# Kernel optimization log

Hardware: AMD Instinct MI355X
Metric: run time of the kernel (lower is better)

## Reference

```python
import jax, jax.numpy as jnp
import numpy as np

B = 1_000_000   # reflections
K = 16_384      # groups
E = 64          # encoder_out
H = 64          # hidden_dim


def setup_inputs() -> dict:
    key = jax.random.key(0)
    ks = jax.random.split(key, 12)
    x = jax.random.normal(ks[0], (B, E), dtype=jnp.float32)
    gl = jax.random.randint(ks[1], (B,), 0, K)
    # guarantee every group id 0..K-1 appears, so torch.unique == arange(K)
    gl = gl.at[:K].set(jnp.arange(K))
    s = 0.05
    W1 = jax.random.normal(ks[2], (E, H), jnp.float32) * s
    b1 = jax.random.normal(ks[3], (H,), jnp.float32) * s
    W2 = jax.random.normal(ks[4], (H, H), jnp.float32) * s
    b2 = jax.random.normal(ks[5], (H,), jnp.float32) * s
    W3 = jax.random.normal(ks[6], (H, H), jnp.float32) * s
    b3 = jax.random.normal(ks[7], (H,), jnp.float32) * s
    w_mu = jax.random.normal(ks[8], (H, 1), jnp.float32) * s
    b_mu = jnp.full((1,), -6.9, jnp.float32)   # log_tau_init
    w_lv = jax.random.normal(ks[9], (H, 1), jnp.float32) * s
    b_lv = jnp.full((1,), -2.0, jnp.float32)
    return {"x": x, "group_labels": gl, "W1": W1, "b1": b1, "W2": W2, "b2": b2,
            "W3": W3, "b3": b3, "w_mu": w_mu, "b_mu": b_mu, "w_lv": w_lv, "b_lv": b_lv}


def reference(x, group_labels, W1, b1, W2, b2, W3, b3, w_mu, b_mu, w_lv, b_lv):
    # phi: Linear -> SiLU -> Linear -> SiLU
    z = jax.nn.silu(jax.nn.silu(x @ W1 + b1) @ W2 + b2)          # (B, H)
    # segment mean by group (math-equivalent to the dense one-hot matmul)
    counts = jax.ops.segment_sum(jnp.ones((z.shape[0],), z.dtype),
                                 group_labels, num_segments=K)    # (K,)
    gsum = jax.ops.segment_sum(z, group_labels, num_segments=K)   # (K, H)
    group_features = gsum / counts[:, None]
    # rho + heads
    h = jax.nn.silu(group_features @ W3 + b3)                     # (K, H)
    mu = (h @ w_mu + b_mu)[:, 0]                                  # (K,)
    logvar = jnp.clip((h @ w_lv + b_lv)[:, 0], -10.0, 4.0)        # (K,)
    std = jnp.exp(0.5 * logvar)
    eps = jax.random.normal(jax.random.key(42), std.shape, std.dtype)
    log_tau = mu + std * eps                                      # reparam sample
    tau_group = jnp.exp(log_tau)
    # unique_groups == arange(K) by construction -> searchsorted is identity
    tau_per_refl = tau_group[group_labels][:, None]               # (B, 1)
    log_tau_per_refl = log_tau[group_labels][:, None]             # (B, 1)
    return (mu, logvar, tau_per_refl, log_tau_per_refl)
```

## Files before the change

kernel.cpp:

```cpp
#include <hip/hip_runtime.h>

#define BN 1000000
#define KN 16384
#define HN 64

typedef __bf16 bf16x8 __attribute__((ext_vector_type(8)));
typedef float  f32x4  __attribute__((ext_vector_type(4)));
typedef unsigned short u16x8 __attribute__((ext_vector_type(8)));

__device__ __forceinline__ unsigned short f2bf(float f) {
    unsigned u = __float_as_uint(f);
    u += 0x7fffu + ((u >> 16) & 1u);
    return (unsigned short)(u >> 16);
}
__device__ __forceinline__ float bf2f(unsigned short b) {
    return __uint_as_float(((unsigned)b) << 16);
}
__device__ __forceinline__ float silu_f(float v) {
    return v * __builtin_amdgcn_rcpf(1.0f + __expf(-v));
}
__device__ __forceinline__ f32x4 mfma16(bf16x8 a, bf16x8 b, f32x4 c) {
    return __builtin_amdgcn_mfma_f32_16x16x32_bf16(a, b, c, 0, 0, 0);
}

__device__ __forceinline__ float erfinv_xla(float x) {
    float w = -log1pf(-x * x);
    float p;
    if (w < 5.0f) {
        w -= 2.5f;
        p = 2.81022636e-08f;
        p = fmaf(p, w, 3.43273939e-07f);
        p = fmaf(p, w, -3.5233877e-06f);
        p = fmaf(p, w, -4.39150654e-06f);
        p = fmaf(p, w, 0.00021858087f);
        p = fmaf(p, w, -0.00125372503f);
        p = fmaf(p, w, -0.00417768164f);
        p = fmaf(p, w, 0.246640727f);
        p = fmaf(p, w, 1.50140941f);
    } else {
        w = sqrtf(w) - 3.0f;
        p = -0.000200214257f;
        p = fmaf(p, w, 0.000100950558f);
        p = fmaf(p, w, 0.00134934322f);
        p = fmaf(p, w, -0.00367342844f);
        p = fmaf(p, w, 0.00573950773f);
        p = fmaf(p, w, -0.0076224613f);
        p = fmaf(p, w, 0.00943887047f);
        p = fmaf(p, w, 1.00167406f);
        p = fmaf(p, w, 2.83297682f);
    }
    return p * x;
}

__device__ __forceinline__ float jax_eps16384(int gid) {
    const unsigned k0 = 0u, k1 = 42u, k2 = 0x1BD11BDAu ^ 0u ^ 42u;
    unsigned x0 = 0u + k0;
    unsigned x1 = (unsigned)gid + k1;
#define TF_RND(r) { x0 += x1; x1 = (x1 << (r)) | (x1 >> (32 - (r))); x1 ^= x0; }
    TF_RND(13) TF_RND(15) TF_RND(26) TF_RND(6)  x0 += k1; x1 += k2 + 1u;
    TF_RND(17) TF_RND(29) TF_RND(16) TF_RND(24) x0 += k2; x1 += k0 + 2u;
    TF_RND(13) TF_RND(15) TF_RND(26) TF_RND(6)  x0 += k0; x1 += k1 + 3u;
    TF_RND(17) TF_RND(29) TF_RND(16) TF_RND(24) x0 += k1; x1 += k2 + 4u;
    TF_RND(13) TF_RND(15) TF_RND(26) TF_RND(6)  x0 += k2; x1 += k0 + 5u;
#undef TF_RND
    unsigned bits = x0 ^ x1;
    float f = __uint_as_float((bits >> 9) | 0x3f800000u) - 1.0f;
    const float mn = -0.99999994f;
    float u = fmaxf(f * 2.0f + mn, mn);
    return 1.41421354f * erfinv_xla(u);
}

__global__ __launch_bounds__(256) void k_count(const int* __restrict__ gl, int* __restrict__ counts) {
    int i = blockIdx.x * 256 + threadIdx.x;
    if (i < BN) atomicAdd(&counts[gl[i]], 1);
}

__global__ __launch_bounds__(1024) void k_scan(const int* __restrict__ counts, int* __restrict__ cursor) {
    __shared__ int part[1024];
    int t = threadIdx.x;
    int loc[16]; int s = 0;
    #pragma unroll
    for (int i = 0; i < 16; ++i) { loc[i] = s; s += counts[t * 16 + i]; }
    part[t] = s;
    __syncthreads();
    for (int off = 1; off < 1024; off <<= 1) {
        int v = (t >= off) ? part[t - off] : 0;
        __syncthreads();
        part[t] += v;
        __syncthreads();
    }
    int base = (t > 0) ? part[t - 1] : 0;
    #pragma unroll
    for (int i = 0; i < 16; ++i) cursor[t * 16 + i] = base + loc[i];
}

__global__ __launch_bounds__(256) void k_scatter(const int* __restrict__ gl, int* __restrict__ cursor,
                                                 int2* __restrict__ spk) {
    int i = blockIdx.x * 256 + threadIdx.x;
    if (i < BN) {
        int g = gl[i];
        int p = atomicAdd(&cursor[g], 1);
        spk[p] = make_int2(i, g);
    }
}

__global__ __launch_bounds__(256) void k_phase1(
    const float* __restrict__ x, const int2* __restrict__ spk,
    const float* __restrict__ W1, const float* __restrict__ b1,
    const float* __restrict__ W2, const float* __restrict__ b2,
    float* __restrict__ gsum)
{
    __shared__ __align__(16) unsigned short w1t[64 * 64];
    __shared__ __align__(16) unsigned short w2t[64 * 64];
    __shared__ __align__(16) unsigned short xh[4][64 * 64];
    __shared__ float b1s[64], b2s[64];
    __shared__ __align__(16) int sg_s[256];

    const int t = threadIdx.x;
    const int base = blockIdx.x * 256;
    const int t4 = t >> 4;
    const int kc = (t & 15) * 4;

    int   rid0[8];
    float4 xv0[8];
    #pragma unroll
    for (int i = 0; i < 8; ++i) {
        int r = base + i * 16 + t4;
        rid0[i] = (r < BN) ? spk[r].x : -1;
    }
    #pragma unroll
    for (int i = 0; i < 8; ++i)
        xv0[i] = (rid0[i] >= 0) ? *(const float4*)(x + (size_t)rid0[i] * 64 + kc)
                                : make_float4(0.f, 0.f, 0.f, 0.f);

    {
        const float4* W1v = (const float4*)W1;
        const float4* W2v = (const float4*)W2;
        #pragma unroll
        for (int i = 0; i < 4; ++i) {
            int e4 = i * 256 + t;
            int k  = e4 >> 4;
            int j0 = (e4 & 15) * 4;
            float4 a = W1v[e4];
            float4 b = W2v[e4];
            float av[4] = {a.x, a.y, a.z, a.w};
            float bv[4] = {b.x, b.y, b.z, b.w};
            #pragma unroll
            for (int c = 0; c < 4; ++c) {
                int j = j0 + c;
                int off = j * 128 + ((2 * k) ^ ((j & 7) << 4));
                *(unsigned short*)((char*)w1t + off) = f2bf(av[c]);
                *(unsigned short*)((char*)w2t + off) = f2bf(bv[c]);
            }
        }
    }

    #pragma unroll
    for (int i = 0; i < 8; ++i) {
        int rr = i * 16 + t4;
        int w = rr >> 6, lr = rr & 63;
        int off = lr * 128 + ((2 * kc) ^ ((lr & 7) << 4));
        ushort4 pk;
        pk.x = f2bf(xv0[i].x); pk.y = f2bf(xv0[i].y);
        pk.z = f2bf(xv0[i].z); pk.w = f2bf(xv0[i].w);
        *(ushort4*)((char*)&xh[w][0] + off) = pk;
    }

    int   rid1[8];
    float4 xv1[8];
    #pragma unroll
    for (int i = 0; i < 8; ++i) {
        int r = base + (8 + i) * 16 + t4;
        rid1[i] = (r < BN) ? spk[r].x : -1;
    }
    #pragma unroll
    for (int i = 0; i < 8; ++i)
        xv1[i] = (rid1[i] >= 0) ? *(const float4*)(x + (size_t)rid1[i] * 64 + kc)
                                : make_float4(0.f, 0.f, 0.f, 0.f);

    if (t < 64) { b1s[t] = b1[t]; b2s[t] = b2[t]; }
    {
        int r = base + t;
        sg_s[t] = (r < BN) ? spk[r].y : -1;
    }

    #pragma unroll
    for (int i = 0; i < 8; ++i) {
        int rr = (8 + i) * 16 + t4;
        int w = rr >> 6, lr = rr & 63;
        int off = lr * 128 + ((2 * kc) ^ ((lr & 7) << 4));
        ushort4 pk;
        pk.x = f2bf(xv1[i].x); pk.y = f2bf(xv1[i].y);
        pk.z = f2bf(xv1[i].z); pk.w = f2bf(xv1[i].w);
        *(ushort4*)((char*)&xh[w][0] + off) = pk;
    }
    __syncthreads();

    const int wv = t >> 6, lane = t & 63;
    const int lj = lane & 15, lg = lane >> 4;
    unsigned short* myx = &xh[wv][0];

    f32x4 acc[4][4];
    #pragma unroll
    for (int a = 0; a < 4; ++a)
        #pragma unroll
        for (int b = 0; b < 4; ++b) acc[a][b] = f32x4{0.f, 0.f, 0.f, 0.f};

    #pragma unroll
    for (int kk = 0; kk < 2; ++kk) {
        const int kbyte = kk * 64 + lg * 16;
        bf16x8 bw[4];
        #pragma unroll
        for (int ct = 0; ct < 4; ++ct) {
            int row = ct * 16 + lj;
            bw[ct] = *(const bf16x8*)((char*)w1t + row * 128 + (kbyte ^ ((row & 7) << 4)));
        }
        #pragma unroll
        for (int rt = 0; rt < 4; ++rt) {
            int row = rt * 16 + lj;
            bf16x8 aw = *(const bf16x8*)((char*)myx + row * 128 + (kbyte ^ ((row & 7) << 4)));
            #pragma unroll
            for (int ct = 0; ct < 4; ++ct)
                acc[rt][ct] = mfma16(aw, bw[ct], acc[rt][ct]);
        }
    }
    {
        float bc[4];
        #pragma unroll
        for (int ct = 0; ct < 4; ++ct) bc[ct] = b1s[ct * 16 + lj];
        #pragma unroll
        for (int rt = 0; rt < 4; ++rt) {
            #pragma unroll
            for (int ct = 0; ct < 4; ++ct) {
                f32x4 v = acc[rt][ct];
                #pragma unroll
                for (int rg = 0; rg < 4; ++rg) {
                    int row = rt * 16 + lg * 4 + rg;
                    int col = ct * 16 + lj;
                    float h = silu_f(v[rg] + bc[ct]);
                    int off = row * 128 + ((2 * col) ^ ((row & 7) << 4));
                    *(unsigned short*)((char*)myx + off) = f2bf(h);
                }
                acc[rt][ct] = f32x4{0.f, 0.f, 0.f, 0.f};
            }
        }
    }
    __syncthreads();

    #pragma unroll
    for (int kk = 0; kk < 2; ++kk) {
        const int kbyte = kk * 64 + lg * 16;
        bf16x8 bw[4];
        #pragma unroll
        for (int ct = 0; ct < 4; ++ct) {
            int row = ct * 16 + lj;
            bw[ct] = *(const bf16x8*)((char*)w2t + row * 128 + (kbyte ^ ((row & 7) << 4)));
        }
        #pragma unroll
        for (int rt = 0; rt < 4; ++rt) {
            int row = rt * 16 + lj;
            bf16x8 aw = *(const bf16x8*)((char*)myx + row * 128 + (kbyte ^ ((row & 7) << 4)));
            #pragma unroll
            for (int ct = 0; ct < 4; ++ct)
                acc[rt][ct] = mfma16(aw, bw[ct], acc[rt][ct]);
        }
    }
    {
        float bc[4];
        #pragma unroll
        for (int ct = 0; ct < 4; ++ct) bc[ct] = b2s[ct * 16 + lj];
        #pragma unroll
        for (int rt = 0; rt < 4; ++rt) {
            #pragma unroll
            for (int ct = 0; ct < 4; ++ct) {
                f32x4 v = acc[rt][ct];
                int col  = ct * 16 + lj;
                int row0 = rt * 16 + lg * 4;
                ushort4 pk;
                pk.x = f2bf(silu_f(v[0] + bc[ct]));
                pk.y = f2bf(silu_f(v[1] + bc[ct]));
                pk.z = f2bf(silu_f(v[2] + bc[ct]));
                pk.w = f2bf(silu_f(v[3] + bc[ct]));
                *(ushort4*)((char*)myx + col * 128 + ((2 * row0) ^ ((col & 7) << 4))) = pk;
            }
        }
    }

    {
        const int c  = t & 63;
        const int ch = t >> 6;
        const char* zT = (const char*)&xh[ch][0];
        float vsum = 0.0f;
        int curg = -2;
        #pragma unroll
        for (int blk = 0; blk < 8; ++blk) {
            u16x8 v = *(const u16x8*)(zT + c * 128 + ((16 * blk) ^ ((c & 7) << 4)));
            int4 ga = *(const int4*)(&sg_s[ch * 64 + blk * 8]);
            int4 gb = *(const int4*)(&sg_s[ch * 64 + blk * 8 + 4]);
            int gs[8] = {ga.x, ga.y, ga.z, ga.w, gb.x, gb.y, gb.z, gb.w};
            #pragma unroll
            for (int j = 0; j < 8; ++j) {
                int g = gs[j];
                if (g != curg) {
                    if (curg >= 0) atomicAdd(&gsum[curg * 64 + c], vsum);
                    vsum = 0.0f;
                    curg = g;
                }
                vsum += bf2f(v[j]);
            }
        }
        if (curg >= 0) atomicAdd(&gsum[curg * 64 + c], vsum);
    }
}

__global__ __launch_bounds__(64) void k_phase2(
    const float* __restrict__ gsum, const int* __restrict__ counts,
    const float* __restrict__ W3, const float* __restrict__ b3,
    const float* __restrict__ wmu, const float* __restrict__ bmu,
    const float* __restrict__ wlv, const float* __restrict__ blv,
    float* __restrict__ out, float* __restrict__ taug, float* __restrict__ ltaug)
{
    __shared__ __align__(16) float w3t[64 * 64];
    __shared__ float b3s[64], wmus[64], wlvs[64];
    const int t = threadIdx.x;
    for (int i = 0; i < 64; ++i) w3t[t * 64 + i] = W3[i * 64 + t];
    b3s[t] = b3[t]; wmus[t] = wmu[t]; wlvs[t] = wlv[t];
    __syncthreads();

    const int gid = blockIdx.x * 64 + t;
    const float inv = 1.0f / (float)counts[gid];
    float gf[64];
    #pragma unroll
    for (int i = 0; i < 16; ++i) {
        float4 v = *(const float4*)(gsum + (size_t)gid * 64 + i * 4);
        gf[i * 4 + 0] = v.x * inv; gf[i * 4 + 1] = v.y * inv;
        gf[i * 4 + 2] = v.z * inv; gf[i * 4 + 3] = v.w * inv;
    }
    float mu = bmu[0], lv = blv[0];
    for (int j = 0; j < 64; ++j) {
        float a = b3s[j];
        const float4* wr = (const float4*)(w3t + j * 64);
        #pragma unroll
        for (int k = 0; k < 16; ++k) {
            float4 wv = wr[k];
            a += gf[k * 4 + 0] * wv.x + gf[k * 4 + 1] * wv.y
               + gf[k * 4 + 2] * wv.z + gf[k * 4 + 3] * wv.w;
        }
        float h = silu_f(a);
        mu += h * wmus[j];
        lv += h * wlvs[j];
    }
    lv = fminf(fmaxf(lv, -10.0f), 4.0f);
    float sd  = __expf(0.5f * lv);
    float eps = jax_eps16384(gid);
    float lt  = mu + sd * eps;
    out[gid]      = mu;
    out[KN + gid] = lv;
    taug[gid]  = __expf(lt);
    ltaug[gid] = lt;
}

__global__ __launch_bounds__(256) void k_phase3(
    const int* __restrict__ gl, const float* __restrict__ taug,
    const float* __restrict__ ltaug, float* __restrict__ out)
{
    int i = blockIdx.x * 256 + threadIdx.x;
    if (i < BN) {
        int g = gl[i];
        out[2 * KN + i]      = taug[g];
        out[2 * KN + BN + i] = ltaug[g];
    }
}

extern "C" void kernel_launch(void* const* d_in, const int* in_sizes, int n_in,
                              void* d_out, int out_size, void* d_ws, size_t ws_size,
                              hipStream_t stream)
{
    const float* x   = (const float*)d_in[0];
    const int*   gl  = (const int*)d_in[1];
    const float* W1  = (const float*)d_in[2];
    const float* b1  = (const float*)d_in[3];
    const float* W2  = (const float*)d_in[4];
    const float* b2  = (const float*)d_in[5];
    const float* W3  = (const float*)d_in[6];
    const float* b3  = (const float*)d_in[7];
    const float* wmu = (const float*)d_in[8];
    const float* bmu = (const float*)d_in[9];
    const float* wlv = (const float*)d_in[10];
    const float* blv = (const float*)d_in[11];
    float* out = (float*)d_out;

    float* ws     = (float*)d_ws;
    float* gsum   = ws;
    int*   counts = (int*)(gsum + KN * HN);
    int*   cursor = counts + KN;
    float* taug   = (float*)(cursor + KN);
    float* ltaug  = taug + KN;
    int2*  spk    = (int2*)(ltaug + KN);

    hipMemsetAsync(gsum, 0, (size_t)KN * HN * sizeof(float), stream);
    hipMemsetAsync(counts, 0, (size_t)KN * sizeof(int), stream);

    const int nb = (BN + 255) / 256;
    k_count  <<<nb, 256, 0, stream>>>(gl, counts);
    k_scan   <<<1, 1024, 0, stream>>>(counts, cursor);
    k_scatter<<<nb, 256, 0, stream>>>(gl, cursor, spk);
    k_phase1 <<<nb, 256, 0, stream>>>(x, spk, W1, b1, W2, b2, gsum);
    k_phase2 <<<KN / 64, 64, 0, stream>>>(gsum, counts, W3, b3, wmu, bmu, wlv, blv, out, taug, ltaug);
    k_phase3 <<<nb, 256, 0, stream>>>(gl, taug, ltaug, out);
}
```

Before: 241.9 us.

## Vectorize index kernels, fold gsum zeroing, load A fragments directly in phase1

```diff
diff --git a/kernel.cpp b/kernel.cpp
--- a/kernel.cpp
+++ b/kernel.cpp
@@ -3,6 +3,8 @@
 #define BN 1000000
 #define KN 16384
 #define HN 64
+#define TPB 384
+#define NW  6
 
 typedef __bf16 bf16x8 __attribute__((ext_vector_type(8)));
 typedef float  f32x4  __attribute__((ext_vector_type(4)));
@@ -70,41 +72,65 @@
     return 1.41421354f * erfinv_xla(u);
 }
 
-__global__ __launch_bounds__(256) void k_count(const int* __restrict__ gl, int* __restrict__ counts) {
+__global__ __launch_bounds__(256) void k_count(const int* __restrict__ gl,
+                                               int* __restrict__ counts,
+                                               float4* __restrict__ gz) {
     int i = blockIdx.x * 256 + threadIdx.x;
-    if (i < BN) atomicAdd(&counts[gl[i]], 1);
+    const float4 z4 = make_float4(0.f, 0.f, 0.f, 0.f);
+    for (int j = i; j < KN * HN / 4; j += 250112) gz[j] = z4;
+    if (i < BN / 4) {
+        int4 g = ((const int4*)gl)[i];
+        atomicAdd(&counts[g.x], 1); atomicAdd(&counts[g.y], 1);
+        atomicAdd(&counts[g.z], 1); atomicAdd(&counts[g.w], 1);
+    }
 }
 
 __global__ __launch_bounds__(1024) void k_scan(const int* __restrict__ counts, int* __restrict__ cursor) {
-    __shared__ int part[1024];
-    int t = threadIdx.x;
-    int loc[16]; int s = 0;
-    #pragma unroll
-    for (int i = 0; i < 16; ++i) { loc[i] = s; s += counts[t * 16 + i]; }
-    part[t] = s;
+    __shared__ int wtot[16];
+    const int t = threadIdx.x, lane = t & 63, wv = t >> 6;
+    const int4* c4 = (const int4*)counts;
+    int4 q0 = c4[t * 4], q1 = c4[t * 4 + 1], q2 = c4[t * 4 + 2], q3 = c4[t * 4 + 3];
+    int c[16] = {q0.x, q0.y, q0.z, q0.w, q1.x, q1.y, q1.z, q1.w,
+                 q2.x, q2.y, q2.z, q2.w, q3.x, q3.y, q3.z, q3.w};
+    int loc[16], s = 0;
+    #pragma unroll
+    for (int i = 0; i < 16; ++i) { loc[i] = s; s += c[i]; }
+    const int own = s;
+    #pragma unroll
+    for (int off = 1; off < 64; off <<= 1) {
+        int v = __shfl_up(s, off);
+        if (lane >= off) s += v;
+    }
+    if (lane == 63) wtot[wv] = s;
     __syncthreads();
-    for (int off = 1; off < 1024; off <<= 1) {
-        int v = (t >= off) ? part[t - off] : 0;
-        __syncthreads();
-        part[t] += v;
-        __syncthreads();
-    }
-    int base = (t > 0) ? part[t - 1] : 0;
-    #pragma unroll
-    for (int i = 0; i < 16; ++i) cursor[t * 16 + i] = base + loc[i];
+    int wbase = 0;
+    #pragma unroll
+    for (int w = 0; w < 16; ++w) wbase += (w < wv) ? wtot[w] : 0;
+    const int ebase = wbase + s - own;
+    int o[16];
+    #pragma unroll
+    for (int i = 0; i < 16; ++i) o[i] = ebase + loc[i];
+    int4* o4 = (int4*)cursor;
+    o4[t * 4]     = make_int4(o[0],  o[1],  o[2],  o[3]);
+    o4[t * 4 + 1] = make_int4(o[4],  o[5],  o[6],  o[7]);
+    o4[t * 4 + 2] = make_int4(o[8],  o[9],  o[10], o[11]);
+    o4[t * 4 + 3] = make_int4(o[12], o[13], o[14], o[15]);
 }
 
 __global__ __launch_bounds__(256) void k_scatter(const int* __restrict__ gl, int* __restrict__ cursor,
                                                  int2* __restrict__ spk) {
     int i = blockIdx.x * 256 + threadIdx.x;
-    if (i < BN) {
-        int g = gl[i];
-        int p = atomicAdd(&cursor[g], 1);
-        spk[p] = make_int2(i, g);
-    }
-}
-
-__global__ __launch_bounds__(256) void k_phase1(
+    if (i < BN / 4) {
+        int4 g = ((const int4*)gl)[i];
+        int r = i * 4;
+        int p0 = atomicAdd(&cursor[g.x], 1); spk[p0] = make_int2(r,     g.x);
+        int p1 = atomicAdd(&cursor[g.y], 1); spk[p1] = make_int2(r + 1, g.y);
+        int p2 = atomicAdd(&cursor[g.z], 1); spk[p2] = make_int2(r + 2, g.z);
+        int p3 = atomicAdd(&cursor[g.w], 1); spk[p3] = make_int2(r + 3, g.w);
+    }
+}
+
+__global__ __launch_bounds__(TPB, 3) void k_phase1(
     const float* __restrict__ x, const int2* __restrict__ spk,
     const float* __restrict__ W1, const float* __restrict__ b1,
     const float* __restrict__ W2, const float* __restrict__ b2,
@@ -112,39 +138,49 @@
 {
     __shared__ __align__(16) unsigned short w1t[64 * 64];
     __shared__ __align__(16) unsigned short w2t[64 * 64];
-    __shared__ __align__(16) unsigned short xh[4][64 * 64];
+    __shared__ __align__(16) unsigned short xh[NW][64 * 64];
     __shared__ float b1s[64], b2s[64];
-    __shared__ __align__(16) int sg_s[256];
+    __shared__ __align__(16) int sg_s[TPB];
 
     const int t = threadIdx.x;
-    const int base = blockIdx.x * 256;
-    const int t4 = t >> 4;
-    const int kc = (t & 15) * 4;
-
-    int   rid0[8];
-    float4 xv0[8];
-    #pragma unroll
-    for (int i = 0; i < 8; ++i) {
-        int r = base + i * 16 + t4;
-        rid0[i] = (r < BN) ? spk[r].x : -1;
-    }
-    #pragma unroll
-    for (int i = 0; i < 8; ++i)
-        xv0[i] = (rid0[i] >= 0) ? *(const float4*)(x + (size_t)rid0[i] * 64 + kc)
-                                : make_float4(0.f, 0.f, 0.f, 0.f);
-
-    {
-        const float4* W1v = (const float4*)W1;
-        const float4* W2v = (const float4*)W2;
-        #pragma unroll
-        for (int i = 0; i < 4; ++i) {
-            int e4 = i * 256 + t;
+    const int wv = t >> 6, lane = t & 63;
+    const int lj = lane & 15, lg = lane >> 4;
+    const int base  = blockIdx.x * TPB;
+    const int wbase = base + wv * 64;
+
+    const float4* W1v = (const float4*)W1;
+    const float4* W2v = (const float4*)W2;
+    float4 wa[3], wb[3];
+    #pragma unroll
+    for (int i = 0; i < 3; ++i) {
+        int e4 = i * TPB + t;
+        if (e4 < 1024) { wa[i] = W1v[e4]; wb[i] = W2v[e4]; }
+    }
+
+    int rid[4];
+    #pragma unroll
+    for (int rt = 0; rt < 4; ++rt) {
+        int r = wbase + rt * 16 + lj;
+        rid[rt] = (r < BN) ? spk[r].x : 0;
+    }
+    float4 xr[4][4];
+    #pragma unroll
+    for (int rt = 0; rt < 4; ++rt) {
+        const float* xp = x + (size_t)rid[rt] * 64 + lg * 8;
+        xr[rt][0] = *(const float4*)(xp);
+        xr[rt][1] = *(const float4*)(xp + 4);
+        xr[rt][2] = *(const float4*)(xp + 32);
+        xr[rt][3] = *(const float4*)(xp + 36);
+    }
+
+    #pragma unroll
+    for (int i = 0; i < 3; ++i) {
+        int e4 = i * TPB + t;
+        if (e4 < 1024) {
             int k  = e4 >> 4;
             int j0 = (e4 & 15) * 4;
-            float4 a = W1v[e4];
-            float4 b = W2v[e4];
-            float av[4] = {a.x, a.y, a.z, a.w};
-            float bv[4] = {b.x, b.y, b.z, b.w};
+            float av[4] = {wa[i].x, wa[i].y, wa[i].z, wa[i].w};
+            float bv[4] = {wb[i].x, wb[i].y, wb[i].z, wb[i].w};
             #pragma unroll
             for (int c = 0; c < 4; ++c) {
                 int j = j0 + c;
@@ -154,50 +190,22 @@
             }
         }
     }
-
-    #pragma unroll
-    for (int i = 0; i < 8; ++i) {
-        int rr = i * 16 + t4;
-        int w = rr >> 6, lr = rr & 63;
-        int off = lr * 128 + ((2 * kc) ^ ((lr & 7) << 4));
-        ushort4 pk;
-        pk.x = f2bf(xv0[i].x); pk.y = f2bf(xv0[i].y);
-        pk.z = f2bf(xv0[i].z); pk.w = f2bf(xv0[i].w);
-        *(ushort4*)((char*)&xh[w][0] + off) = pk;
-    }
-
-    int   rid1[8];
-    float4 xv1[8];
-    #pragma unroll
-    for (int i = 0; i < 8; ++i) {
-        int r = base + (8 + i) * 16 + t4;
-        rid1[i] = (r < BN) ? spk[r].x : -1;
-    }
-    #pragma unroll
-    for (int i = 0; i < 8; ++i)
-        xv1[i] = (rid1[i] >= 0) ? *(const float4*)(x + (size_t)rid1[i] * 64 + kc)
-                                : make_float4(0.f, 0.f, 0.f, 0.f);
-
     if (t < 64) { b1s[t] = b1[t]; b2s[t] = b2[t]; }
-    {
-        int r = base + t;
-        sg_s[t] = (r < BN) ? spk[r].y : -1;
-    }
-
-    #pragma unroll
-    for (int i = 0; i < 8; ++i) {
-        int rr = (8 + i) * 16 + t4;
-        int w = rr >> 6, lr = rr & 63;
-        int off = lr * 128 + ((2 * kc) ^ ((lr & 7) << 4));
-        ushort4 pk;
-        pk.x = f2bf(xv1[i].x); pk.y = f2bf(xv1[i].y);
-        pk.z = f2bf(xv1[i].z); pk.w = f2bf(xv1[i].w);
-        *(ushort4*)((char*)&xh[w][0] + off) = pk;
-    }
+    sg_s[t] = (base + t < BN) ? spk[base + t].y : -1;
     __syncthreads();
 
-    const int wv = t >> 6, lane = t & 63;
-    const int lj = lane & 15, lg = lane >> 4;
+    bf16x8 af[4][2];
+    #pragma unroll
+    for (int rt = 0; rt < 4; ++rt)
+        #pragma unroll
+        for (int kk = 0; kk < 2; ++kk) {
+            float4 a = xr[rt][kk * 2], b = xr[rt][kk * 2 + 1];
+            u16x8 u;
+            u[0] = f2bf(a.x); u[1] = f2bf(a.y); u[2] = f2bf(a.z); u[3] = f2bf(a.w);
+            u[4] = f2bf(b.x); u[5] = f2bf(b.y); u[6] = f2bf(b.z); u[7] = f2bf(b.w);
+            af[rt][kk] = __builtin_bit_cast(bf16x8, u);
+        }
+
     unsigned short* myx = &xh[wv][0];
 
     f32x4 acc[4][4];
@@ -216,13 +224,10 @@
             bw[ct] = *(const bf16x8*)((char*)w1t + row * 128 + (kbyte ^ ((row & 7) << 4)));
         }
         #pragma unroll
-        for (int rt = 0; rt < 4; ++rt) {
-            int row = rt * 16 + lj;
-            bf16x8 aw = *(const bf16x8*)((char*)myx + row * 128 + (kbyte ^ ((row & 7) << 4)));
+        for (int rt = 0; rt < 4; ++rt)
             #pragma unroll
             for (int ct = 0; ct < 4; ++ct)
-                acc[rt][ct] = mfma16(aw, bw[ct], acc[rt][ct]);
-        }
+                acc[rt][ct] = mfma16(af[rt][kk], bw[ct], acc[rt][ct]);
     }
     {
         float bc[4];
@@ -245,7 +250,6 @@
             }
         }
     }
-    __syncthreads();
 
     #pragma unroll
     for (int kk = 0; kk < 2; ++kk) {
@@ -287,16 +291,15 @@
     }
 
     {
-        const int c  = t & 63;
-        const int ch = t >> 6;
-        const char* zT = (const char*)&xh[ch][0];
+        const int c  = lane;
+        const char* zT = (const char*)myx;
         float vsum = 0.0f;
         int curg = -2;
         #pragma unroll
         for (int blk = 0; blk < 8; ++blk) {
             u16x8 v = *(const u16x8*)(zT + c * 128 + ((16 * blk) ^ ((c & 7) << 4)));
-            int4 ga = *(const int4*)(&sg_s[ch * 64 + blk * 8]);
-            int4 gb = *(const int4*)(&sg_s[ch * 64 + blk * 8 + 4]);
+            int4 ga = *(const int4*)(&sg_s[wv * 64 + blk * 8]);
+            int4 gb = *(const int4*)(&sg_s[wv * 64 + blk * 8 + 4]);
             int gs[8] = {ga.x, ga.y, ga.z, ga.w, gb.x, gb.y, gb.z, gb.w};
             #pragma unroll
             for (int j = 0; j < 8; ++j) {
@@ -365,10 +368,12 @@
     const float* __restrict__ ltaug, float* __restrict__ out)
 {
     int i = blockIdx.x * 256 + threadIdx.x;
-    if (i < BN) {
-        int g = gl[i];
-        out[2 * KN + i]      = taug[g];
-        out[2 * KN + BN + i] = ltaug[g];
+    if (i < BN / 4) {
+        int4 g = ((const int4*)gl)[i];
+        float4 tv = make_float4(taug[g.x],  taug[g.y],  taug[g.z],  taug[g.w]);
+        float4 lv = make_float4(ltaug[g.x], ltaug[g.y], ltaug[g.z], ltaug[g.w]);
+        ((float4*)(out + 2 * KN))[i]      = tv;
+        ((float4*)(out + 2 * KN + BN))[i] = lv;
     }
 }
 
@@ -398,14 +403,14 @@
     float* ltaug  = taug + KN;
     int2*  spk    = (int2*)(ltaug + KN);
 
-    hipMemsetAsync(gsum, 0, (size_t)KN * HN * sizeof(float), stream);
     hipMemsetAsync(counts, 0, (size_t)KN * sizeof(int), stream);
 
-    const int nb = (BN + 255) / 256;
-    k_count  <<<nb, 256, 0, stream>>>(gl, counts);
+    const int nb4 = (BN / 4 + 255) / 256;
+    const int nb1 = (BN + TPB - 1) / TPB;
+    k_count  <<<nb4, 256, 0, stream>>>(gl, counts, (float4*)gsum);
     k_scan   <<<1, 1024, 0, stream>>>(counts, cursor);
-    k_scatter<<<nb, 256, 0, stream>>>(gl, cursor, spk);
-    k_phase1 <<<nb, 256, 0, stream>>>(x, spk, W1, b1, W2, b2, gsum);
+    k_scatter<<<nb4, 256, 0, stream>>>(gl, cursor, spk);
+    k_phase1 <<<nb1, TPB, 0, stream>>>(x, spk, W1, b1, W2, b2, gsum);
     k_phase2 <<<KN / 64, 64, 0, stream>>>(gsum, counts, W3, b3, wmu, bmu, wlv, blv, out, taug, ltaug);
-    k_phase3 <<<nb, 256, 0, stream>>>(gl, taug, ltaug, out);
-}
+    k_phase3 <<<nb4, 256, 0, stream>>>(gl, taug, ltaug, out);
+}
```

Measured after the change: 263.1 us. +8.7%, slower.
